# Kernel tuning notes

Hardware: AMD Instinct MI355X
Metric: run time of the kernel (lower is better)

## Reference

```python
import math
import jax, jax.numpy as jnp
import numpy as np

EPS = 1e-5
THETA = 2.0 ** 16


def ln(x):
    # parameter-free LayerNorm over last dim (biased variance, like torch)
    m = jnp.mean(x, axis=-1, keepdims=True)
    v = jnp.mean((x - m) ** 2, axis=-1, keepdims=True)
    return (x - m) / jnp.sqrt(v + EPS)


def get_freqs(n):
    # quantize(arange(n), 2): floor to even so adjacent pairs share a frequency
    t = jnp.floor(jnp.arange(n, dtype=jnp.float32) / 2.0) * 2.0
    return 1.0 / (THETA ** (t / n)) / (2.0 * math.pi)


def rope(cos, sin, v):
    # v: (B, nh, T, N); cos/sin: (T, N) broadcast
    v_rot = jnp.stack((-v[..., 1::2], v[..., ::2]), axis=-1).reshape(v.shape)
    return v * cos + v_rot * sin


def setup_inputs() -> dict:
    key = jax.random.key(0)
    ks = jax.random.split(key, 6)
    B, T, D, nh, N, V = 2, 2048, 256, 4, 4096, 256
    std = 0.02
    return {
        "idx": jax.random.randint(ks[0], (B, T), 0, V, dtype=jnp.int64 if jax.config.jax_enable_x64 else jnp.int32),
        "embed": jax.random.normal(ks[1], (V, D), jnp.float32) * std,
        "encoder": jax.random.normal(ks[2], (nh, D, N), jnp.float32) * std,
        "encoder_v": jax.random.normal(ks[3], (nh, D, N), jnp.float32) * std,
        "decoder": jax.random.normal(ks[4], (nh * N, D), jnp.float32) * std,
        "lm_head": jax.random.normal(ks[5], (D, V), jnp.float32) * std,
    }


def reference(idx, embed, encoder, encoder_v, decoder, lm_head):
    n_layer = 6
    B, T = idx.shape
    nh, D, N = encoder.shape[0], encoder.shape[1], encoder.shape[2]
    dec = decoder.reshape(nh, N, D)

    # RoPE phase tables (t_offset = 0)
    freqs = get_freqs(N)                                   # (N,)
    phases = jnp.arange(T, dtype=jnp.float32)[:, None] * freqs[None, :]
    ph = (phases % 1.0) * (2.0 * math.pi)
    cos, sin = jnp.cos(ph), jnp.sin(ph)                    # (T, N)

    # strictly-lower causal mask (tril, diagonal=-1)
    mask = jnp.tril(jnp.ones((T, T), dtype=bool), k=-1)

    x = ln(jnp.take(embed, idx, axis=0))                   # (B, T, D)

    for _ in range(n_layer):
        x_latent = jnp.einsum("btd,hdn->bhtn", x, encoder)
        x_sparse = jax.nn.relu(x_latent)                   # (B, nh, T, N)

        QR = rope(cos, sin, x_sparse)
        KR = rope(cos, sin, x_sparse)
        scores = jnp.einsum("bhtn,bhsn->bhts", QR, KR)
        scores = jnp.where(mask, scores, 0.0)
        yKV = jnp.einsum("bhts,bsd->bhtd", scores, x)      # V = x broadcast over heads

        yKV = ln(yKV)
        y_sparse = jax.nn.relu(jnp.einsum("bhtd,hdn->bhtn", yKV, encoder_v))
        xy_sparse = x_sparse * y_sparse                    # gated sparse activations
        yMLP = jnp.einsum("bhtn,hnd->btd", xy_sparse, dec)
        x = ln(x + ln(yMLP))

    logits = jnp.einsum("btd,dv->btv", x, lm_head)
    return logits
```

## Files before the change

kernel.cpp:

```cpp
#include <hip/hip_runtime.h>


typedef unsigned short u16;
typedef unsigned int   u32;
typedef __attribute__((ext_vector_type(8))) short bf8;
typedef __attribute__((ext_vector_type(4))) float f4;

#define T_  2048
#define D_  256
#define NH_ 4
#define NN_ 4096
#define NLAYER 6

#define XB_E   524288u
#define QR_E   33554432u
#define QR_U32 16777216u
#define SP_U16 8912896u
#define SP_U32 4456448u
#define SP_F   4456448u
#define YKV_F  2097152u
#define YKH_E  2097152u

#define CSA_OFF  ((size_t)0)
#define CSB_OFF  (CSA_OFF  + 262144)
#define ETH_OFF  (CSB_OFF  + 2097152)
#define EVH_OFF  (ETH_OFF  + 8388608)
#define DTH_OFF  (EVH_OFF  + 8388608)
#define LMH_OFF  (DTH_OFF  + 8388608)
#define LML_OFF  (LMH_OFF  + 131072)
#define X_OFF    (LML_OFF  + 131072)
#define XBH_OFF  (X_OFF    + 4194304)
#define XBL_OFF  (XBH_OFF  + 2097152)
#define XBTH_OFF (XBL_OFF  + 2097152)
#define QRH_OFF  (XBTH_OFF + 2097152)
#define SH_OFF   (QRH_OFF  + 134217728)
#define YKV_OFF  (SH_OFF   + 35651584)
#define YKH_OFF  (YKV_OFF  + 16777216)
#define WS_NEED  (YKH_OFF  + 8388608)

__device__ __forceinline__ u16 f2b(float f) {
  u32 u = __builtin_bit_cast(u32, f);
  u32 r = u + 0x7fffu + ((u >> 16) & 1u);
  return (u16)(r >> 16);
}
__device__ __forceinline__ float b2f(u16 h) {
  u32 u = ((u32)h) << 16;
  return __builtin_bit_cast(float, u);
}
__device__ __forceinline__ float wsum(float v) {
#pragma unroll
  for (int o = 32; o; o >>= 1) v += __shfl_xor(v, o, 64);
  return v;
}
__device__ __forceinline__ float2 trig_ct(const float2* csA, const float2* csB, int t, int pp) {
  float2 a = csA[(t >> 7) * 2048 + pp];
  float2 b = csB[(t & 127) * 2048 + pp];
  return make_float2(a.x * b.x - a.y * b.y, a.x * b.y + a.y * b.x);
}
__device__ __forceinline__ void gld16(const u16* g, short* l) {
  __builtin_amdgcn_global_load_lds(
      (const __attribute__((address_space(1))) u32*)g,
      (__attribute__((address_space(3))) u32*)l, 16, 0, 0);
}
__device__ __forceinline__ void stage_t(const u16* g, int lda, short* s, int wid, int lane) {
  int r8 = lane >> 3;
  int c8 = ((lane & 7) ^ r8) * 8;
#pragma unroll
  for (int j = 0; j < 4; ++j) {
    int row = wid * 32 + j * 8;
    gld16(g + (size_t)(row + r8) * lda + c8, s + row * 64);
  }
}
__device__ __forceinline__ void stage_t8(const u16* g, int lda, short* s, int wid, int lane) {
  int r8 = lane >> 3;
  int c8 = ((lane & 7) ^ r8) * 8;
#pragma unroll
  for (int j = 0; j < 2; ++j) {
    int row = wid * 16 + j * 8;
    gld16(g + (size_t)(row + r8) * lda + c8, s + row * 64);
  }
}
__device__ __forceinline__ void mma64x3(const short* AsH, const short* AsL, const short* BsH,
                                        const short* BsL, int wr, int wc, int lane,
                                        f4 acc[4][4]) {
  int r15 = lane & 15, hi = lane >> 4;
  int sw = (r15 & 7) << 3;
#pragma unroll
  for (int kk = 0; kk < 2; ++kk) {
    int ko = (kk * 32 + hi * 8) ^ sw;
    bf8 ah[4], al[4], bh[4], bl[4];
#pragma unroll
    for (int m = 0; m < 4; ++m) {
      int off = (wr * 64 + m * 16 + r15) * 64 + ko;
      ah[m] = *(const bf8*)(AsH + off);
      al[m] = *(const bf8*)(AsL + off);
    }
#pragma unroll
    for (int n = 0; n < 4; ++n) {
      int off = (wc * 64 + n * 16 + r15) * 64 + ko;
      bh[n] = *(const bf8*)(BsH + off);
      bl[n] = *(const bf8*)(BsL + off);
    }
#pragma unroll
    for (int m = 0; m < 4; ++m)
#pragma unroll
      for (int n = 0; n < 4; ++n) {
        acc[m][n] = __builtin_amdgcn_mfma_f32_16x16x32_bf16(ah[m], bh[n], acc[m][n], 0, 0, 0);
        acc[m][n] = __builtin_amdgcn_mfma_f32_16x16x32_bf16(al[m], bh[n], acc[m][n], 0, 0, 0);
        acc[m][n] = __builtin_amdgcn_mfma_f32_16x16x32_bf16(ah[m], bl[n], acc[m][n], 0, 0, 0);
      }
  }
}
__device__ __forceinline__ void mma64x1(const short* AsH, const short* BsH,
                                        int wr, int wc, int lane, f4 acc[4][4]) {
  int r15 = lane & 15, hi = lane >> 4;
  int sw = (r15 & 7) << 3;
#pragma unroll
  for (int kk = 0; kk < 2; ++kk) {
    int ko = (kk * 32 + hi * 8) ^ sw;
    bf8 ah[4], bh[4];
#pragma unroll
    for (int m = 0; m < 4; ++m)
      ah[m] = *(const bf8*)(AsH + (wr * 64 + m * 16 + r15) * 64 + ko);
#pragma unroll
    for (int n = 0; n < 4; ++n)
      bh[n] = *(const bf8*)(BsH + (wc * 64 + n * 16 + r15) * 64 + ko);
#pragma unroll
    for (int m = 0; m < 4; ++m)
#pragma unroll
      for (int n = 0; n < 4; ++n)
        acc[m][n] = __builtin_amdgcn_mfma_f32_16x16x32_bf16(ah[m], bh[n], acc[m][n], 0, 0, 0);
  }
}
__device__ __forceinline__ void acc_zero(f4 acc[4][4]) {
#pragma unroll
  for (int m = 0; m < 4; ++m)
#pragma unroll
    for (int n = 0; n < 4; ++n)
#pragma unroll
      for (int j = 0; j < 4; ++j) acc[m][n][j] = 0.0f;
}
__device__ __forceinline__ void acc_store_f32(float* F, f4 acc[4][4], int wr, int wc, int lane,
                                              bool relu) {
  int r15 = lane & 15, q = lane >> 4;
#pragma unroll
  for (int m = 0; m < 4; ++m)
#pragma unroll
    for (int n = 0; n < 4; ++n)
#pragma unroll
      for (int j = 0; j < 4; ++j) {
        float v = acc[m][n][j];
        if (relu) v = fmaxf(v, 0.0f);
        F[(wr * 64 + m * 16 + q * 4 + j) * 128 + wc * 64 + n * 16 + r15] = v;
      }
}
__device__ __forceinline__ void acc_store_half(float* F, f4 acc[4][4], int pass, int wr, int wc,
                                               int lane, bool relu) {
  if (wr != pass) return;
  int r15 = lane & 15, q = lane >> 4;
#pragma unroll
  for (int m = 0; m < 4; ++m)
#pragma unroll
    for (int n = 0; n < 4; ++n)
#pragma unroll
      for (int j = 0; j < 4; ++j) {
        float v = acc[m][n][j];
        if (relu) v = fmaxf(v, 0.0f);
        F[(m * 16 + q * 4 + j) * 128 + wc * 64 + n * 16 + r15] = v;
      }
}

__global__ __launch_bounds__(256) void k_costab(float2* csA, float2* csB) {
  int id = blockIdx.x * 256 + threadIdx.x;
  int r = id >> 11, p = id & 2047;
  double freq = exp2(-(double)p / 128.0) * 0.15915494309189533577;
  int t = (r < 16) ? (r * 128) : (r - 16);
  double ph = fmod((double)t * freq, 1.0);
  double ang = ph * 6.2831853071795864769;
  float2 v = make_float2((float)cos(ang), (float)sin(ang));
  if (r < 16) csA[r * 2048 + p] = v;
  else        csB[(r - 16) * 2048 + p] = v;
}

__global__ __launch_bounds__(256) void k_tcast1(const float* __restrict__ in,
                                                u16* __restrict__ outH, int R, int C) {
  __shared__ float tl[32][33];
  size_t bo = (size_t)blockIdx.z * R * C;
  int tx = threadIdx.x, ty = threadIdx.y;
  int c = blockIdx.x * 32 + tx, r0 = blockIdx.y * 32 + ty;
#pragma unroll
  for (int k = 0; k < 32; k += 8) tl[ty + k][tx] = in[bo + (size_t)(r0 + k) * C + c];
  __syncthreads();
  int rr = blockIdx.y * 32 + tx, cc0 = blockIdx.x * 32 + ty;
#pragma unroll
  for (int k = 0; k < 32; k += 8) outH[bo + (size_t)(cc0 + k) * R + rr] = f2b(tl[tx][ty + k]);
}

__global__ __launch_bounds__(256) void k_tcast2(const float* __restrict__ in,
                                                u16* __restrict__ outH, u16* __restrict__ outL,
                                                int R, int C) {
  __shared__ float tl[32][33];
  int tx = threadIdx.x, ty = threadIdx.y;
  int c = blockIdx.x * 32 + tx, r0 = blockIdx.y * 32 + ty;
#pragma unroll
  for (int k = 0; k < 32; k += 8) tl[ty + k][tx] = in[(size_t)(r0 + k) * C + c];
  __syncthreads();
  int rr = blockIdx.y * 32 + tx, cc0 = blockIdx.x * 32 + ty;
#pragma unroll
  for (int k = 0; k < 32; k += 8) {
    float v = tl[tx][ty + k];
    u16 h = f2b(v);
    outH[(size_t)(cc0 + k) * R + rr] = h;
    outL[(size_t)(cc0 + k) * R + rr] = f2b(v - b2f(h));
  }
}

__global__ __launch_bounds__(256) void k_ln_embed(const int* __restrict__ idx,
                                                  const float* __restrict__ embed,
                                                  float* __restrict__ x, u16* __restrict__ xbH,
                                                  u16* __restrict__ xbL) {
  int lane = threadIdx.x & 63, wid = threadIdx.x >> 6;
  int r = blockIdx.x * 4 + wid;
  int id = idx[r] & 255;
  float4 v = ((const float4*)(embed + (size_t)id * 256))[lane];
  float m = wsum(v.x + v.y + v.z + v.w) * (1.0f / 256.0f);
  float d0 = v.x - m, d1 = v.y - m, d2 = v.z - m, d3 = v.w - m;
  float var = wsum(d0 * d0 + d1 * d1 + d2 * d2 + d3 * d3) * (1.0f / 256.0f);
  float rs = 1.0f / sqrtf(var + 1e-5f);
  float y0 = d0 * rs, y1 = d1 * rs, y2 = d2 * rs, y3 = d3 * rs;
  ((float4*)(x + (size_t)r * 256))[lane] = make_float4(y0, y1, y2, y3);
  ushort4 oh, ol;
  oh.x = f2b(y0); ol.x = f2b(y0 - b2f(oh.x));
  oh.y = f2b(y1); ol.y = f2b(y1 - b2f(oh.y));
  oh.z = f2b(y2); ol.z = f2b(y2 - b2f(oh.z));
  oh.w = f2b(y3); ol.w = f2b(y3 - b2f(oh.w));
  ((ushort4*)(xbH + (size_t)r * 256))[lane] = oh;
  ((ushort4*)(xbL + (size_t)r * 256))[lane] = ol;
}

__global__ __launch_bounds__(256) void k_xbt(const u16* __restrict__ xbH,
                                             u16* __restrict__ xbTH) {
  int id = blockIdx.x * 256 + threadIdx.x;
  int b = id >> 19;
  int w19 = id & 524287;
  int t = w19 & 2047, d = w19 >> 11;
  xbTH[id] = xbH[(size_t)b * XB_E + (size_t)t * 256 + d];
}

#define GEMM_PRE1                                                       \
  __shared__ short sm1[16384];                                          \
  short* T0 = sm1;                                                      \
  short* T1 = sm1 + 8192;                                               \
  float* bounce = (float*)sm1;                                          \
  int tid = threadIdx.x;                                                \
  int lane = tid & 63, wid = tid >> 6;                                  \
  int wr = wid >> 1, wc = wid & 1;                                      \
  f4 acc[4][4];                                                         \
  acc_zero(acc);

#define GEMM_PRE1D                                                      \
  __shared__ short smd1[32768];                                         \
  float* bounce = (float*)smd1;                                         \
  int tid = threadIdx.x;                                                \
  int lane = tid & 63, wid = tid >> 6;                                  \
  int wr = wid >> 1, wc = wid & 1;                                      \
  f4 acc[4][4];                                                         \
  acc_zero(acc);

__global__ __launch_bounds__(256) void k_g1(const u16* __restrict__ xbH,
                                            const u16* __restrict__ etH,
                                            const float2* __restrict__ csA,
                                            const float2* __restrict__ csB,
                                            u16* __restrict__ QRH) {
  GEMM_PRE1
  int it = blockIdx.x, jt = blockIdx.y;
  int h = blockIdx.z & 3, bb = blockIdx.z >> 2;
  size_t ao = (size_t)bb * XB_E + (size_t)it * 128 * 256;
  size_t bo = (size_t)h * NN_ * 256 + (size_t)jt * 128 * 256;
  for (int kb = 0; kb < 4; ++kb) {
    stage_t(xbH + ao + kb * 64, 256, T0, wid, lane);
    stage_t(etH + bo + kb * 64, 256, T1, wid, lane);
    __syncthreads();
    mma64x1(T0, T1, wr, wc, lane, acc);
    __syncthreads();
  }
#pragma unroll
  for (int pass = 0; pass < 2; ++pass) {
    acc_store_half(bounce, acc, pass, wr, wc, lane, true);
    __syncthreads();
    for (int w = 0; w < 16; ++w) {
      int e = w * 256 + tid;
      int rrel = e >> 6, p = e & 63;
      float v0 = bounce[rrel * 128 + 2 * p], v1 = bounce[rrel * 128 + 2 * p + 1];
      int t = it * 128 + pass * 64 + rrel, pp = jt * 64 + p;
      float2 c = trig_ct(csA, csB, t, pp);
      float q0 = v0 * c.x - v1 * c.y;
      float q1 = v1 * c.x + v0 * c.y;
      u32 hi = (u32)f2b(q0) | ((u32)f2b(q1) << 16);
      ((u32*)QRH)[(size_t)bb * QR_U32 + (size_t)(h * T_ + t) * 2048 + pp] = hi;
    }
    __syncthreads();
  }
}

__global__ __launch_bounds__(512) void k_g2(const u16* __restrict__ QRH,
                                            u16* __restrict__ SpH) {
  __shared__ short smp[65536];
  float* bounce = (float*)smp;
  int tid = threadIdx.x;
  int lane = tid & 63, wid = tid >> 6;
  int wr = wid >> 2, wc = wid & 3;
  f4 acc[4][6];
#pragma unroll
  for (int m = 0; m < 4; ++m)
#pragma unroll
    for (int n = 0; n < 6; ++n)
#pragma unroll
      for (int j = 0; j < 4; ++j) acc[m][n][j] = 0.0f;
  int orig = blockIdx.x;
  int lb = (orig & 7) * 51 + (orig >> 3);
  int bb = lb / 204;
  int l2 = lb % 204;
  int h = l2 / 51;
  int rem = l2 % 51, i = 0;
  while (rem >= (i + 3) / 3) { rem -= (i + 3) / 3; ++i; }
  int j0 = rem * 3, j1 = j0 + 1, j2 = j0 + 2;
  bool has1 = (j1 <= i), has2 = (j2 <= i);
  size_t base = (size_t)bb * QR_E + (size_t)h * T_ * NN_;
  size_t ao = base + (size_t)i * 128 * NN_;
  size_t bo0 = base + (size_t)j0 * 128 * NN_;
  size_t bo1 = base + (size_t)j1 * 128 * NN_;
  size_t bo2 = base + (size_t)j2 * 128 * NN_;
  {
    stage_t8(QRH + ao, NN_, smp, wid, lane);
    stage_t8(QRH + bo0, NN_, smp + 8192, wid, lane);
    if (has1) stage_t8(QRH + bo1, NN_, smp + 16384, wid, lane);
    if (has2) stage_t8(QRH + bo2, NN_, smp + 24576, wid, lane);
  }
  int r15 = lane & 15, hi4 = lane >> 4;
  int sw = (r15 & 7) << 3;
  for (int kb = 0; kb < 64; ++kb) {
    short* cur = smp + (kb & 1) * 32768;
    __syncthreads();
    if (kb + 1 < 64) {
      short* nxt = smp + ((kb + 1) & 1) * 32768;
      stage_t8(QRH + ao + (kb + 1) * 64, NN_, nxt, wid, lane);
      stage_t8(QRH + bo0 + (kb + 1) * 64, NN_, nxt + 8192, wid, lane);
      if (has1) stage_t8(QRH + bo1 + (kb + 1) * 64, NN_, nxt + 16384, wid, lane);
      if (has2) stage_t8(QRH + bo2 + (kb + 1) * 64, NN_, nxt + 24576, wid, lane);
    }
#pragma unroll
    for (int kk = 0; kk < 2; ++kk) {
      int ko = (kk * 32 + hi4 * 8) ^ sw;
      bf8 ah[4];
#pragma unroll
      for (int m = 0; m < 4; ++m)
        ah[m] = *(const bf8*)(cur + (wr * 64 + m * 16 + r15) * 64 + ko);
#pragma unroll
      for (int n = 0; n < 6; ++n) {
        int cn = wc * 96 + n * 16;
        int bp = cn >> 7;
        if (bp == 1 && !has1) continue;
        if (bp == 2 && !has2) continue;
        bf8 bh = *(const bf8*)(cur + 8192 + bp * 8192 + ((cn & 127) + r15) * 64 + ko);
#pragma unroll
        for (int m = 0; m < 4; ++m)
          acc[m][n] = __builtin_amdgcn_mfma_f32_16x16x32_bf16(ah[m], bh, acc[m][n], 0, 0, 0);
      }
    }
  }
  __syncthreads();
  int q4 = lane >> 4;
#pragma unroll
  for (int jb = 0; jb < 3; ++jb) {
    if (jb == 1 && !has1) break;
    if (jb == 2 && !has2) break;
    int j = j0 + jb;
    size_t dblk = ((size_t)h * 136 + (size_t)i * (i + 1) / 2 + j) * 16384;
    bool diag = (i == j);
#pragma unroll
    for (int pass = 0; pass < 2; ++pass) {
      if (wr == pass) {
#pragma unroll
        for (int m = 0; m < 4; ++m)
#pragma unroll
          for (int n = 0; n < 6; ++n) {
            int cn = wc * 96 + n * 16;
            if ((cn >> 7) != jb) continue;
#pragma unroll
            for (int jj = 0; jj < 4; ++jj)
              bounce[(m * 16 + q4 * 4 + jj) * 128 + (cn & 127) + r15] = acc[m][n][jj];
          }
      }
      __syncthreads();
      for (int w = 0; w < 8; ++w) {
        int e = w * 512 + tid;
        int rrel = e >> 6, p = e & 63;
        int row = pass * 64 + rrel;
        float s0 = bounce[rrel * 128 + 2 * p], s1 = bounce[rrel * 128 + 2 * p + 1];
        if (diag) {
          if (2 * p >= row) s0 = 0.0f;
          if (2 * p + 1 >= row) s1 = 0.0f;
        }
        u32 hi = (u32)f2b(s0) | ((u32)f2b(s1) << 16);
        ((u32*)SpH)[(size_t)bb * SP_U32 + (dblk >> 1) + row * 64 + p] = hi;
      }
      __syncthreads();
    }
  }
}

__global__ __launch_bounds__(256) void k_g3(const u16* __restrict__ SpH,
                                            const u16* __restrict__ xbTH,
                                            float* __restrict__ yKV) {
  GEMM_PRE1D
  int i = blockIdx.x, jt = blockIdx.y;
  int h = blockIdx.z & 3, bb = blockIdx.z >> 2;
  size_t tri = (size_t)bb * 544 + (size_t)h * 136 + (size_t)i * (i + 1) / 2;
  size_t bo = (size_t)bb * XB_E + (size_t)jt * 128 * T_;
  int nk = 2 * (i + 1);
  {
    stage_t(SpH + tri * 16384, 128, smd1, wid, lane);
    stage_t(xbTH + bo, T_, smd1 + 8192, wid, lane);
  }
  for (int kb = 0; kb < nk; ++kb) {
    short* cur = smd1 + (kb & 1) * 16384;
    __syncthreads();
    if (kb + 1 < nk) {
      short* nxt = smd1 + ((kb + 1) & 1) * 16384;
      size_t aoff = (tri + ((kb + 1) >> 1)) * 16384 + ((kb + 1) & 1) * 64;
      stage_t(SpH + aoff, 128, nxt, wid, lane);
      stage_t(xbTH + bo + (kb + 1) * 64, T_, nxt + 8192, wid, lane);
    }
    mma64x1(cur, cur + 8192, wr, wc, lane, acc);
  }
  __syncthreads();
#pragma unroll
  for (int pass = 0; pass < 2; ++pass) {
    acc_store_half(bounce, acc, pass, wr, wc, lane, false);
    __syncthreads();
    for (int w = 0; w < 32; ++w) {
      int e = w * 256 + tid;
      int row = e >> 7, col = e & 127;
      yKV[(size_t)bb * YKV_F + ((size_t)h * T_ + i * 128 + pass * 64 + row) * 256 + jt * 128 + col] =
          bounce[row * 128 + col];
    }
    __syncthreads();
  }
}

__global__ __launch_bounds__(256) void k_ln_f32(const float* __restrict__ in,
                                                u16* __restrict__ outH) {
  int lane = threadIdx.x & 63, wid = threadIdx.x >> 6;
  int r = blockIdx.x * 4 + wid;
  float4 v = ((const float4*)(in + (size_t)r * 256))[lane];
  float m = wsum(v.x + v.y + v.z + v.w) * (1.0f / 256.0f);
  float d0 = v.x - m, d1 = v.y - m, d2 = v.z - m, d3 = v.w - m;
  float var = wsum(d0 * d0 + d1 * d1 + d2 * d2 + d3 * d3) * (1.0f / 256.0f);
  float rs = 1.0f / sqrtf(var + 1e-5f);
  ushort4 oh;
  oh.x = f2b(d0 * rs); oh.y = f2b(d1 * rs); oh.z = f2b(d2 * rs); oh.w = f2b(d3 * rs);
  ((ushort4*)(outH + (size_t)r * 256))[lane] = oh;
}

__global__ __launch_bounds__(256) void k_g4a(const u16* __restrict__ ykH,
                                             const u16* __restrict__ evH,
                                             const float2* __restrict__ csA,
                                             const float2* __restrict__ csB,
                                             u16* __restrict__ QRH) {
  GEMM_PRE1
  int it = blockIdx.x, jt = blockIdx.y;
  int h = blockIdx.z & 3, bb = blockIdx.z >> 2;
  int t0 = it * 128;
  size_t ao = (size_t)bb * YKH_E + (size_t)(h * T_ + t0) * 256;
  size_t bo = (size_t)h * NN_ * 256 + (size_t)jt * 128 * 256;
  for (int kb = 0; kb < 4; ++kb) {
    stage_t(ykH + ao + kb * 64, 256, T0, wid, lane);
    stage_t(evH + bo + kb * 64, 256, T1, wid, lane);
    __syncthreads();
    mma64x1(T0, T1, wr, wc, lane, acc);
    __syncthreads();
  }
#pragma unroll
  for (int pass = 0; pass < 2; ++pass) {
    acc_store_half(bounce, acc, pass, wr, wc, lane, true);
    __syncthreads();
    for (int w = 0; w < 16; ++w) {
      int e = w * 256 + tid;
      int rrel = e >> 6, p = e & 63;
      float ys0 = bounce[rrel * 128 + 2 * p], ys1 = bounce[rrel * 128 + 2 * p + 1];
      int t = t0 + pass * 64 + rrel, pp = jt * 64 + p;
      size_t u32b = (size_t)bb * QR_U32 + (size_t)(h * T_ + t) * 2048 + pp;
      u32 qh = ((const u32*)QRH)[u32b];
      float qe = b2f((u16)(qh & 0xffff));
      float qo = b2f((u16)(qh >> 16));
      float2 c = trig_ct(csA, csB, t, pp);
      float xe = fmaxf(qe * c.x + qo * c.y, 0.0f);
      float xo = fmaxf(qo * c.x - qe * c.y, 0.0f);
      u32 hi = (u32)f2b(ys0 * xe) | ((u32)f2b(ys1 * xo) << 16);
      ((u32*)QRH)[u32b] = hi;
    }
    __syncthreads();
  }
}

__global__ __launch_bounds__(256) void k_g4b(const u16* __restrict__ xyH,
                                             const u16* __restrict__ dtH,
                                             float* __restrict__ part) {
  GEMM_PRE1D
  int it = blockIdx.x, jt = blockIdx.y;
  int h = blockIdx.z & 3, ks = (blockIdx.z >> 2) & 1, bb = blockIdx.z >> 3;
  int z8 = h + 4 * ks;
  int t0 = it * 128;
  size_t ao = (size_t)bb * QR_E + (size_t)(h * T_ + t0) * NN_;
  size_t bo = (size_t)h * D_ * NN_ + (size_t)jt * 128 * NN_;
  int k0 = ks * 32, k1 = ks * 32 + 32;
  {
    stage_t(xyH + ao + k0 * 64, NN_, smd1, wid, lane);
    stage_t(dtH + bo + k0 * 64, NN_, smd1 + 8192, wid, lane);
  }
  for (int kb = k0; kb < k1; ++kb) {
    short* cur = smd1 + ((kb - k0) & 1) * 16384;
    __syncthreads();
    if (kb + 1 < k1) {
      short* nxt = smd1 + ((kb + 1 - k0) & 1) * 16384;
      stage_t(xyH + ao + (kb + 1) * 64, NN_, nxt, wid, lane);
      stage_t(dtH + bo + (kb + 1) * 64, NN_, nxt + 8192, wid, lane);
    }
    mma64x1(cur, cur + 8192, wr, wc, lane, acc);
  }
  __syncthreads();
#pragma unroll
  for (int pass = 0; pass < 2; ++pass) {
    acc_store_half(bounce, acc, pass, wr, wc, lane, false);
    __syncthreads();
    for (int w = 0; w < 32; ++w) {
      int e = w * 256 + tid;
      int row = e >> 7, col = e & 127;
      part[(size_t)bb * SP_F + ((size_t)z8 * T_ + t0 + pass * 64 + row) * 256 + jt * 128 + col] =
          bounce[row * 128 + col];
    }
    __syncthreads();
  }
}

__global__ __launch_bounds__(256) void k_ln3(const float* __restrict__ part, float* __restrict__ x,
                                             u16* __restrict__ xbH, u16* __restrict__ xbL) {
  int lane = threadIdx.x & 63, wid = threadIdx.x >> 6;
  int r = blockIdx.x * 4 + wid;
  int bb = r >> 11, rl = r & 2047;
  const float* P = part + (size_t)bb * SP_F;
  float a0 = 0, a1 = 0, a2 = 0, a3 = 0;
#pragma unroll
  for (int h = 0; h < 8; ++h) {
    float4 u = ((const float4*)(P + ((size_t)h * T_ + rl) * 256))[lane];
    a0 += u.x; a1 += u.y; a2 += u.z; a3 += u.w;
  }
  float m = wsum(a0 + a1 + a2 + a3) * (1.0f / 256.0f);
  float d0 = a0 - m, d1 = a1 - m, d2 = a2 - m, d3 = a3 - m;
  float var = wsum(d0 * d0 + d1 * d1 + d2 * d2 + d3 * d3) * (1.0f / 256.0f);
  float rs = 1.0f / sqrtf(var + 1e-5f);
  float4 xv = ((const float4*)(x + (size_t)r * 256))[lane];
  float s0 = xv.x + d0 * rs, s1 = xv.y + d1 * rs, s2 = xv.z + d2 * rs, s3 = xv.w + d3 * rs;
  float m2 = wsum(s0 + s1 + s2 + s3) * (1.0f / 256.0f);
  float e0 = s0 - m2, e1 = s1 - m2, e2 = s2 - m2, e3 = s3 - m2;
  float var2 = wsum(e0 * e0 + e1 * e1 + e2 * e2 + e3 * e3) * (1.0f / 256.0f);
  float rs2 = 1.0f / sqrtf(var2 + 1e-5f);
  float y0 = e0 * rs2, y1 = e1 * rs2, y2 = e2 * rs2, y3 = e3 * rs2;
  ((float4*)(x + (size_t)r * 256))[lane] = make_float4(y0, y1, y2, y3);
  ushort4 oh, ol;
  oh.x = f2b(y0); ol.x = f2b(y0 - b2f(oh.x));
  oh.y = f2b(y1); ol.y = f2b(y1 - b2f(oh.y));
  oh.z = f2b(y2); ol.z = f2b(y2 - b2f(oh.z));
  oh.w = f2b(y3); ol.w = f2b(y3 - b2f(oh.w));
  ((ushort4*)(xbH + (size_t)r * 256))[lane] = oh;
  ((ushort4*)(xbL + (size_t)r * 256))[lane] = ol;
}

__global__ __launch_bounds__(256) void k_g5(const u16* __restrict__ xbH,
                                            const u16* __restrict__ xbL,
                                            const u16* __restrict__ lmH,
                                            const u16* __restrict__ lmL,
                                            float* __restrict__ out) {
  __shared__ float smf[16384];
  short* AsH = (short*)smf;
  short* AsL = AsH + 8192;
  short* BsH = AsH + 16384;
  short* BsL = AsH + 24576;
  int tid = threadIdx.x;
  int lane = tid & 63, wid = tid >> 6;
  int wr = wid >> 1, wc = wid & 1;
  f4 acc[4][4];
  acc_zero(acc);
  int it = blockIdx.x, jt = blockIdx.y;
  size_t ao = (size_t)it * 128 * 256;
  size_t bo = (size_t)jt * 128 * 256;
  for (int kb = 0; kb < 4; ++kb) {
    stage_t(xbH + ao + kb * 64, 256, AsH, wid, lane);
    stage_t(xbL + ao + kb * 64, 256, AsL, wid, lane);
    stage_t(lmH + bo + kb * 64, 256, BsH, wid, lane);
    stage_t(lmL + bo + kb * 64, 256, BsL, wid, lane);
    __syncthreads();
    mma64x3(AsH, AsL, BsH, BsL, wr, wc, lane, acc);
    __syncthreads();
  }
  acc_store_f32(smf, acc, wr, wc, lane, false);
  __syncthreads();
  for (int w = 0; w < 64; ++w) {
    int e = w * 256 + tid;
    int row = e >> 7, col = e & 127;
    out[(size_t)(it * 128 + row) * 256 + jt * 128 + col] = smf[row * 128 + col];
  }
}

extern "C" void kernel_launch(void* const* d_in, const int* in_sizes, int n_in, void* d_out,
                              int out_size, void* d_ws, size_t ws_size, hipStream_t stream) {
  const int*   idx   = (const int*)d_in[0];
  const float* embed = (const float*)d_in[1];
  const float* enc   = (const float*)d_in[2];
  const float* encv  = (const float*)d_in[3];
  const float* dec   = (const float*)d_in[4];
  const float* lm    = (const float*)d_in[5];

  if (ws_size < WS_NEED) {
    hipMemsetAsync(d_out, 0x46, (size_t)out_size * 4, stream);
    return;
  }

  char* w = (char*)d_ws;
  float2* csA  = (float2*)(w + CSA_OFF);
  float2* csB  = (float2*)(w + CSB_OFF);
  u16*    etH  = (u16*)(w + ETH_OFF);
  u16*    evH  = (u16*)(w + EVH_OFF);
  u16*    dtH  = (u16*)(w + DTH_OFF);
  u16*    lmH  = (u16*)(w + LMH_OFF);
  u16*    lmL  = (u16*)(w + LML_OFF);
  float*  x    = (float*)(w + X_OFF);
  u16*    xbH  = (u16*)(w + XBH_OFF);
  u16*    xbL  = (u16*)(w + XBL_OFF);
  u16*    xbTH = (u16*)(w + XBTH_OFF);
  u16*    QRH  = (u16*)(w + QRH_OFF);
  u16*    SpH  = (u16*)(w + SH_OFF);
  float*  part = (float*)(w + SH_OFF);
  float*  yKV  = (float*)(w + YKV_OFF);
  u16*    ykH  = (u16*)(w + YKH_OFF);

  k_costab<<<1152, 256, 0, stream>>>(csA, csB);
  k_tcast1<<<dim3(128, 8, 4), dim3(32, 8), 0, stream>>>(enc, etH, 256, 4096);
  k_tcast1<<<dim3(128, 8, 4), dim3(32, 8), 0, stream>>>(encv, evH, 256, 4096);
  k_tcast1<<<dim3(8, 128, 4), dim3(32, 8), 0, stream>>>(dec, dtH, 4096, 256);
  k_tcast2<<<dim3(8, 8, 1), dim3(32, 8), 0, stream>>>(lm, lmH, lmL, 256, 256);
  k_ln_embed<<<1024, 256, 0, stream>>>(idx, embed, x, xbH, xbL);
  k_xbt<<<4096, 256, 0, stream>>>(xbH, xbTH);

  for (int l = 0; l < NLAYER; ++l) {
    k_g1<<<dim3(16, 32, 8), 256, 0, stream>>>(xbH, etH, csA, csB, QRH);
    k_g2<<<408, 512, 0, stream>>>(QRH, SpH);
    k_g3<<<dim3(16, 2, 8), 256, 0, stream>>>(SpH, xbTH, yKV);
    k_ln_f32<<<4096, 256, 0, stream>>>(yKV, ykH);
    k_g4a<<<dim3(16, 32, 8), 256, 0, stream>>>(ykH, evH, csA, csB, QRH);
    k_g4b<<<dim3(16, 2, 16), 256, 0, stream>>>(QRH, dtH, part);
    k_ln3<<<1024, 256, 0, stream>>>(part, x, xbH, xbL);
    k_xbt<<<4096, 256, 0, stream>>>(xbH, xbTH);
  }
  k_g5<<<dim3(32, 2), 256, 0, stream>>>(xbH, xbL, lmH, lmL, (float*)d_out);
}
```

Before: 3.022 ms.

## Double-buffer g1/g4a staging and enlarge g2 score tile to 256x384

k_g1 and k_g4a now stage the next K-slice into a second shared buffer while the current one is multiplied, which removes one barrier per iteration and overlaps loads with MFMA. k_g2, the causal QR·QRᵀ score GEMM, now has each block compute two 128-row blocks against up to three column blocks, using 48 accumulators per wave instead of 24. That cuts redundant re-reading of QR rows and halves the grid to 216 blocks. The cost is larger LDS per block (160KB for g2, 64KB for g1/g4a) and higher register pressure, which may lower occupancy, and fewer blocks than CUs could leave some CUs idle.

```diff
diff --git a/kernel.cpp b/kernel.cpp
--- a/kernel.cpp
+++ b/kernel.cpp
@@ -15,7 +15,6 @@
 #define XB_E   524288u
 #define QR_E   33554432u
 #define QR_U32 16777216u
-#define SP_U16 8912896u
 #define SP_U32 4456448u
 #define SP_F   4456448u
 #define YKV_F  2097152u
@@ -247,17 +246,6 @@
   xbTH[id] = xbH[(size_t)b * XB_E + (size_t)t * 256 + d];
 }
 
-#define GEMM_PRE1                                                       \
-  __shared__ short sm1[16384];                                          \
-  short* T0 = sm1;                                                      \
-  short* T1 = sm1 + 8192;                                               \
-  float* bounce = (float*)sm1;                                          \
-  int tid = threadIdx.x;                                                \
-  int lane = tid & 63, wid = tid >> 6;                                  \
-  int wr = wid >> 1, wc = wid & 1;                                      \
-  f4 acc[4][4];                                                         \
-  acc_zero(acc);
-
 #define GEMM_PRE1D                                                      \
   __shared__ short smd1[32768];                                         \
   float* bounce = (float*)smd1;                                         \
@@ -272,18 +260,26 @@
                                             const float2* __restrict__ csA,
                                             const float2* __restrict__ csB,
                                             u16* __restrict__ QRH) {
-  GEMM_PRE1
+  GEMM_PRE1D
   int it = blockIdx.x, jt = blockIdx.y;
   int h = blockIdx.z & 3, bb = blockIdx.z >> 2;
   size_t ao = (size_t)bb * XB_E + (size_t)it * 128 * 256;
   size_t bo = (size_t)h * NN_ * 256 + (size_t)jt * 128 * 256;
+  {
+    stage_t(xbH + ao, 256, smd1, wid, lane);
+    stage_t(etH + bo, 256, smd1 + 8192, wid, lane);
+  }
   for (int kb = 0; kb < 4; ++kb) {
-    stage_t(xbH + ao + kb * 64, 256, T0, wid, lane);
-    stage_t(etH + bo + kb * 64, 256, T1, wid, lane);
-    __syncthreads();
-    mma64x1(T0, T1, wr, wc, lane, acc);
-    __syncthreads();
-  }
+    short* cur = smd1 + (kb & 1) * 16384;
+    __syncthreads();
+    if (kb + 1 < 4) {
+      short* nxt = smd1 + ((kb + 1) & 1) * 16384;
+      stage_t(xbH + ao + (kb + 1) * 64, 256, nxt, wid, lane);
+      stage_t(etH + bo + (kb + 1) * 64, 256, nxt + 8192, wid, lane);
+    }
+    mma64x1(cur, cur + 8192, wr, wc, lane, acc);
+  }
+  __syncthreads();
 #pragma unroll
   for (int pass = 0; pass < 2; ++pass) {
     acc_store_half(bounce, acc, pass, wr, wc, lane, true);
@@ -305,64 +301,69 @@
 
 __global__ __launch_bounds__(512) void k_g2(const u16* __restrict__ QRH,
                                             u16* __restrict__ SpH) {
-  __shared__ short smp[65536];
+  __shared__ short smp[81920];
   float* bounce = (float*)smp;
   int tid = threadIdx.x;
   int lane = tid & 63, wid = tid >> 6;
-  int wr = wid >> 2, wc = wid & 3;
-  f4 acc[4][6];
+  int wr = wid >> 1, wc = wid & 1;
+  f4 acc[4][12];
 #pragma unroll
   for (int m = 0; m < 4; ++m)
 #pragma unroll
-    for (int n = 0; n < 6; ++n)
+    for (int n = 0; n < 12; ++n)
 #pragma unroll
       for (int j = 0; j < 4; ++j) acc[m][n][j] = 0.0f;
   int orig = blockIdx.x;
-  int lb = (orig & 7) * 51 + (orig >> 3);
-  int bb = lb / 204;
-  int l2 = lb % 204;
-  int h = l2 / 51;
-  int rem = l2 % 51, i = 0;
-  while (rem >= (i + 3) / 3) { rem -= (i + 3) / 3; ++i; }
-  int j0 = rem * 3, j1 = j0 + 1, j2 = j0 + 2;
-  bool has1 = (j1 <= i), has2 = (j2 <= i);
+  int lb = (orig & 7) * 27 + (orig >> 3);
+  int bb = lb / 108;
+  int l2 = lb % 108;
+  int h = l2 / 27;
+  int rem = l2 % 27, P = 0;
+  while (rem >= (2 * P + 4) / 3) { rem -= (2 * P + 4) / 3; ++P; }
+  int j0 = rem * 3;
+  int i1 = 2 * P + 1;
+  bool has1 = (j0 + 1 <= i1), has2 = (j0 + 2 <= i1);
   size_t base = (size_t)bb * QR_E + (size_t)h * T_ * NN_;
-  size_t ao = base + (size_t)i * 128 * NN_;
+  size_t ao = base + (size_t)P * 256 * NN_;
   size_t bo0 = base + (size_t)j0 * 128 * NN_;
-  size_t bo1 = base + (size_t)j1 * 128 * NN_;
-  size_t bo2 = base + (size_t)j2 * 128 * NN_;
+  size_t bo1 = base + (size_t)(j0 + 1) * 128 * NN_;
+  size_t bo2 = base + (size_t)(j0 + 2) * 128 * NN_;
   {
     stage_t8(QRH + ao, NN_, smp, wid, lane);
-    stage_t8(QRH + bo0, NN_, smp + 8192, wid, lane);
-    if (has1) stage_t8(QRH + bo1, NN_, smp + 16384, wid, lane);
-    if (has2) stage_t8(QRH + bo2, NN_, smp + 24576, wid, lane);
+    stage_t8(QRH + ao + 128 * NN_, NN_, smp + 8192, wid, lane);
+    stage_t8(QRH + bo0, NN_, smp + 16384, wid, lane);
+    if (has1) stage_t8(QRH + bo1, NN_, smp + 24576, wid, lane);
+    if (has2) stage_t8(QRH + bo2, NN_, smp + 32768, wid, lane);
   }
   int r15 = lane & 15, hi4 = lane >> 4;
   int sw = (r15 & 7) << 3;
   for (int kb = 0; kb < 64; ++kb) {
-    short* cur = smp + (kb & 1) * 32768;
+    short* cur = smp + (kb & 1) * 40960;
     __syncthreads();
     if (kb + 1 < 64) {
-      short* nxt = smp + ((kb + 1) & 1) * 32768;
+      short* nxt = smp + ((kb + 1) & 1) * 40960;
       stage_t8(QRH + ao + (kb + 1) * 64, NN_, nxt, wid, lane);
-      stage_t8(QRH + bo0 + (kb + 1) * 64, NN_, nxt + 8192, wid, lane);
-      if (has1) stage_t8(QRH + bo1 + (kb + 1) * 64, NN_, nxt + 16384, wid, lane);
-      if (has2) stage_t8(QRH + bo2 + (kb + 1) * 64, NN_, nxt + 24576, wid, lane);
+      stage_t8(QRH + ao + 128 * NN_ + (kb + 1) * 64, NN_, nxt + 8192, wid, lane);
+      stage_t8(QRH + bo0 + (kb + 1) * 64, NN_, nxt + 16384, wid, lane);
+      if (has1) stage_t8(QRH + bo1 + (kb + 1) * 64, NN_, nxt + 24576, wid, lane);
+      if (has2) stage_t8(QRH + bo2 + (kb + 1) * 64, NN_, nxt + 32768, wid, lane);
     }
 #pragma unroll
     for (int kk = 0; kk < 2; ++kk) {
       int ko = (kk * 32 + hi4 * 8) ^ sw;
       bf8 ah[4];
 #pragma unroll
-      for (int m = 0; m < 4; ++m)
-        ah[m] = *(const bf8*)(cur + (wr * 64 + m * 16 + r15) * 64 + ko);
-#pragma unroll
-      for (int n = 0; n < 6; ++n) {
-        int cn = wc * 96 + n * 16;
+      for (int m = 0; m < 4; ++m) {
+        int row = wr * 64 + m * 16 + r15;
+        ah[m] = *(const bf8*)(cur + (row >> 7) * 8192 + (row & 127) * 64 + ko);
+      }
+#pragma unroll
+      for (int n = 0; n < 12; ++n) {
+        int cn = wc * 192 + n * 16;
         int bp = cn >> 7;
         if (bp == 1 && !has1) continue;
         if (bp == 2 && !has2) continue;
-        bf8 bh = *(const bf8*)(cur + 8192 + bp * 8192 + ((cn & 127) + r15) * 64 + ko);
+        bf8 bh = *(const bf8*)(cur + 16384 + bp * 8192 + ((cn & 127) + r15) * 64 + ko);
 #pragma unroll
         for (int m = 0; m < 4; ++m)
           acc[m][n] = __builtin_amdgcn_mfma_f32_16x16x32_bf16(ah[m], bh, acc[m][n], 0, 0, 0);
@@ -372,40 +373,43 @@
   __syncthreads();
   int q4 = lane >> 4;
 #pragma unroll
-  for (int jb = 0; jb < 3; ++jb) {
-    if (jb == 1 && !has1) break;
-    if (jb == 2 && !has2) break;
-    int j = j0 + jb;
-    size_t dblk = ((size_t)h * 136 + (size_t)i * (i + 1) / 2 + j) * 16384;
-    bool diag = (i == j);
-#pragma unroll
-    for (int pass = 0; pass < 2; ++pass) {
-      if (wr == pass) {
-#pragma unroll
-        for (int m = 0; m < 4; ++m)
-#pragma unroll
-          for (int n = 0; n < 6; ++n) {
-            int cn = wc * 96 + n * 16;
-            if ((cn >> 7) != jb) continue;
-#pragma unroll
-            for (int jj = 0; jj < 4; ++jj)
-              bounce[(m * 16 + q4 * 4 + jj) * 128 + (cn & 127) + r15] = acc[m][n][jj];
+  for (int ib = 0; ib < 2; ++ib) {
+    int i = 2 * P + ib;
+#pragma unroll
+    for (int jb = 0; jb < 3; ++jb) {
+      int j = j0 + jb;
+      if (j > i) continue;
+      size_t dblk = (size_t)h * 136 + (size_t)i * (i + 1) / 2 + j;
+      bool diag = (i == j);
+#pragma unroll
+      for (int pass = 0; pass < 2; ++pass) {
+        if (wr == 2 * ib + pass) {
+#pragma unroll
+          for (int m = 0; m < 4; ++m)
+#pragma unroll
+            for (int n = 0; n < 12; ++n) {
+              int cn = wc * 192 + n * 16;
+              if ((cn >> 7) != jb) continue;
+#pragma unroll
+              for (int jj = 0; jj < 4; ++jj)
+                bounce[(m * 16 + q4 * 4 + jj) * 128 + (cn & 127) + r15] = acc[m][n][jj];
+            }
+        }
+        __syncthreads();
+        for (int w = 0; w < 8; ++w) {
+          int e = w * 512 + tid;
+          int rrel = e >> 6, p = e & 63;
+          int row = pass * 64 + rrel;
+          float s0 = bounce[rrel * 128 + 2 * p], s1 = bounce[rrel * 128 + 2 * p + 1];
+          if (diag) {
+            if (2 * p >= row) s0 = 0.0f;
+            if (2 * p + 1 >= row) s1 = 0.0f;
           }
+          u32 hi = (u32)f2b(s0) | ((u32)f2b(s1) << 16);
+          ((u32*)SpH)[(size_t)bb * SP_U32 + dblk * 8192 + row * 64 + p] = hi;
+        }
+        __syncthreads();
       }
-      __syncthreads();
-      for (int w = 0; w < 8; ++w) {
-        int e = w * 512 + tid;
-        int rrel = e >> 6, p = e & 63;
-        int row = pass * 64 + rrel;
-        float s0 = bounce[rrel * 128 + 2 * p], s1 = bounce[rrel * 128 + 2 * p + 1];
-        if (diag) {
-          if (2 * p >= row) s0 = 0.0f;
-          if (2 * p + 1 >= row) s1 = 0.0f;
-        }
-        u32 hi = (u32)f2b(s0) | ((u32)f2b(s1) << 16);
-        ((u32*)SpH)[(size_t)bb * SP_U32 + (dblk >> 1) + row * 64 + p] = hi;
-      }
-      __syncthreads();
     }
   }
 }
@@ -468,19 +472,27 @@
                                              const float2* __restrict__ csA,
                                              const float2* __restrict__ csB,
                                              u16* __restrict__ QRH) {
-  GEMM_PRE1
+  GEMM_PRE1D
   int it = blockIdx.x, jt = blockIdx.y;
   int h = blockIdx.z & 3, bb = blockIdx.z >> 2;
   int t0 = it * 128;
   size_t ao = (size_t)bb * YKH_E + (size_t)(h * T_ + t0) * 256;
   size_t bo = (size_t)h * NN_ * 256 + (size_t)jt * 128 * 256;
+  {
+    stage_t(ykH + ao, 256, smd1, wid, lane);
+    stage_t(evH + bo, 256, smd1 + 8192, wid, lane);
+  }
   for (int kb = 0; kb < 4; ++kb) {
-    stage_t(ykH + ao + kb * 64, 256, T0, wid, lane);
-    stage_t(evH + bo + kb * 64, 256, T1, wid, lane);
-    __syncthreads();
-    mma64x1(T0, T1, wr, wc, lane, acc);
-    __syncthreads();
-  }
+    short* cur = smd1 + (kb & 1) * 16384;
+    __syncthreads();
+    if (kb + 1 < 4) {
+      short* nxt = smd1 + ((kb + 1) & 1) * 16384;
+      stage_t(ykH + ao + (kb + 1) * 64, 256, nxt, wid, lane);
+      stage_t(evH + bo + (kb + 1) * 64, 256, nxt + 8192, wid, lane);
+    }
+    mma64x1(cur, cur + 8192, wr, wc, lane, acc);
+  }
+  __syncthreads();
 #pragma unroll
   for (int pass = 0; pass < 2; ++pass) {
     acc_store_half(bounce, acc, pass, wr, wc, lane, true);
@@ -655,7 +667,7 @@
 
   for (int l = 0; l < NLAYER; ++l) {
     k_g1<<<dim3(16, 32, 8), 256, 0, stream>>>(xbH, etH, csA, csB, QRH);
-    k_g2<<<408, 512, 0, stream>>>(QRH, SpH);
+    k_g2<<<216, 512, 0, stream>>>(QRH, SpH);
     k_g3<<<dim3(16, 2, 8), 256, 0, stream>>>(SpH, xbTH, yKV);
     k_ln_f32<<<4096, 256, 0, stream>>>(yKV, ykH);
     k_g4a<<<dim3(16, 32, 8), 256, 0, stream>>>(ykH, evH, csA, csB, QRH);
```

Result: slower. 4.050 ms (+34.0%).
